# Optimization experiments

Hardware: AMD Instinct MI355X
Metric: run time of the kernel (lower is better)

## Reference

```python
import jax, jax.numpy as jnp
import numpy as np
import math

B, S, D, H = 2, 2048, 1024, 16
DK = D // H

def setup_inputs() -> dict:
    key = jax.random.key(0)
    ks = jax.random.split(key, 8)
    query = jax.random.normal(ks[0], (B, S, D), dtype=jnp.float32)
    k_in = jax.random.normal(ks[1], (B, S, D), dtype=jnp.float32)
    value = jax.random.normal(ks[2], (B, S, D), dtype=jnp.float32)
    mask = jax.random.randint(ks[3], (B, S, S), 0, 2, dtype=jnp.int32)
    scale = 1.0 / math.sqrt(D)
    Wq = jax.random.normal(ks[4], (D, D), dtype=jnp.float32) * scale
    Wk = jax.random.normal(ks[5], (D, D), dtype=jnp.float32) * scale
    Wv = jax.random.normal(ks[6], (D, D), dtype=jnp.float32) * scale
    Wo = jax.random.normal(ks[7], (D, D), dtype=jnp.float32) * scale
    return {"query": query, "key": k_in, "value": value, "mask": mask,
            "Wq": Wq, "Wk": Wk, "Wv": Wv, "Wo": Wo}

def reference(query, key, value, mask, Wq, Wk, Wv, Wo):
    # torch Linear(no bias): y = x @ W.T ; weights are [out, in]
    def split_heads(x):  # [B,S,D] -> [B,H,S,DK]
        return x.reshape(B, S, H, DK).transpose(0, 2, 1, 3)
    q = split_heads(query @ Wq.T)
    k = split_heads(key @ Wk.T)
    v = split_heads(value @ Wv.T)
    scores = jnp.einsum('bhqd,bhkd->bhqk', q, k) / jnp.sqrt(jnp.float32(DK))
    scores = jnp.where(mask[:, None, :, :] == 0, jnp.float32(-1e9), scores)
    p_attn = jax.nn.softmax(scores, axis=-1)  # dropout is identity in eval mode
    attn = jnp.einsum('bhqk,bhkd->bhqd', p_attn, v)
    out = attn.transpose(0, 2, 1, 3).reshape(B, S, D)
    return out @ Wo.T
```

## Files before the change

kernel.cpp:

```cpp
#include <hip/hip_runtime.h>
#include <hip/hip_bf16.h>
#include <cstdint>
#include <cstddef>

constexpr int BATCH = 2;
constexpr int SEQ   = 2048;
constexpr int DIM   = 1024;
constexpr int NH    = 16;
constexpr int DK    = 64;

typedef unsigned short u16;
typedef unsigned int   u32;
typedef unsigned long long u64;

typedef __attribute__((ext_vector_type(8))) short bf16x8;
typedef __attribute__((ext_vector_type(8))) unsigned short u16x8;
typedef __attribute__((ext_vector_type(4))) float f32x4;
typedef __attribute__((ext_vector_type(16))) float f32x16;
typedef __attribute__((ext_vector_type(4))) unsigned int u32x4;

__device__ __forceinline__ u16 f2bf(float f) {
  u32 u = __builtin_bit_cast(u32, f);
  u32 r = (u + 0x7FFFu + ((u >> 16) & 1u)) >> 16;
  return (u16)r;
}

__device__ __forceinline__ u32 pack_bf2(float a, float b) {
  __hip_bfloat162 h2 = __float22bfloat162_rn(make_float2(a, b));
  u32 r;
  __builtin_memcpy(&r, &h2, 4);
  return r;
}

__device__ __forceinline__ float fexp2(float x) {
#if __has_builtin(__builtin_amdgcn_exp2f)
  return __builtin_amdgcn_exp2f(x);
#else
  return exp2f(x);
#endif
}

__device__ __forceinline__ void plswap32(u32& a, u32& b) {
  asm volatile("v_permlane32_swap_b32 %0, %1" : "+v"(a), "+v"(b));
}

__device__ __forceinline__ void gload16(const u16* g, u16* l) {
  __builtin_amdgcn_global_load_lds(
      (const __attribute__((address_space(1))) void*)g,
      (__attribute__((address_space(3))) void*)l, 16, 0, 0);
}

constexpr size_t QS  = (size_t)BATCH * SEQ * DIM;
constexpr size_t WSZ = (size_t)DIM * DIM;
constexpr int CVT_BLOCKS  = (int)((3 * QS + 4 * WSZ) / (256 * 8));
constexpr int MASK_BLOCKS = (BATCH * SEQ * SEQ) / 256;

__global__ __launch_bounds__(256) void prep(const float* __restrict__ q,
                                            const float* __restrict__ k,
                                            const float* __restrict__ v,
                                            const float* __restrict__ wq,
                                            const float* __restrict__ wk,
                                            const float* __restrict__ wv,
                                            const float* __restrict__ wo,
                                            u16* __restrict__ dst,
                                            const int* __restrict__ mask,
                                            u64* __restrict__ bits) {
  const int bid = blockIdx.x;
  if (bid < CVT_BLOCKS) {
    const size_t i = ((size_t)bid * 256 + threadIdx.x) * 8;
    const float* s;
    if      (i < QS)              s = q  + i;
    else if (i < 2 * QS)          s = k  + (i - QS);
    else if (i < 3 * QS)          s = v  + (i - 2 * QS);
    else if (i < 3 * QS + WSZ)     s = wq + (i - 3 * QS);
    else if (i < 3 * QS + 2 * WSZ) s = wk + (i - 3 * QS - WSZ);
    else if (i < 3 * QS + 3 * WSZ) s = wv + (i - 3 * QS - 2 * WSZ);
    else                           s = wo + (i - 3 * QS - 3 * WSZ);
    f32x4 a = *(const f32x4*)s, b2 = *(const f32x4*)(s + 4);
    u32x4 t;
    t[0] = pack_bf2(a[0], a[1]);  t[1] = pack_bf2(a[2], a[3]);
    t[2] = pack_bf2(b2[0], b2[1]); t[3] = pack_bf2(b2[2], b2[3]);
    *(u16x8*)(dst + i) = __builtin_bit_cast(u16x8, t);
  } else {
    const int gt = (bid - CVT_BLOCKS) * 256 + threadIdx.x;
    u64 m = __ballot(mask[gt] != 0);
    if ((threadIdx.x & 63) == 0) bits[gt >> 6] = m;
  }
}

__global__ __launch_bounds__(256) void transpose_v(const u16* __restrict__ V,
                                                   u16* __restrict__ Vt) {
  __shared__ u16 t[64][68];
  const int st = blockIdx.x * 64;
  const int bh = blockIdx.y;
  const int b = bh >> 4, h = bh & 15;
  const int tid = threadIdx.x;
#pragma unroll
  for (int s = 0; s < 2; ++s) {
    int c = tid + s * 256;
    int row = c >> 3, c8 = c & 7;
    u16x8 vv = *(const u16x8*)(V + ((size_t)(b * SEQ + st + row)) * DIM + h * DK + c8 * 8);
#pragma unroll
    for (int j = 0; j < 8; ++j) t[row][c8 * 8 + j] = vv[j];
  }
  __syncthreads();
#pragma unroll
  for (int s = 0; s < 2; ++s) {
    int c = tid + s * 256;
    int dk = c >> 3, sc = c & 7;
    u16x8 ov;
#pragma unroll
    for (int j = 0; j < 8; ++j) ov[j] = t[sc * 8 + j][dk];
    *(u16x8*)(Vt + ((size_t)bh * DK + dk) * SEQ + st + sc * 8) = ov;
  }
}

struct GemmParams {
  const void* A[3];
  const void* B[3];
  void*       C[3];
  float       alpha[3];
};

template <bool OUTF32>
__global__ __launch_bounds__(256) void gemm_nt(GemmParams p, int M, int N, int K) {
  const int z = blockIdx.z;
  __shared__ __align__(16) u16 As[128 * 64];
  __shared__ __align__(16) u16 Bs[128 * 64];

  const int nbx = gridDim.x, nby = gridDim.y;
  const int lid = blockIdx.y * nbx + blockIdx.x;
  const int xcd = lid & 7, idx = lid >> 3;
  const int rows_per_xcd = nby >> 3;
  const int by = xcd * rows_per_xcd + idx / nbx;
  const int bx = idx % nbx;

  const int tid = threadIdx.x;
  const int lane = tid & 63, w = tid >> 6;
  const int l31 = lane & 31, hi = lane >> 5;
  const int bm = by * 128, bn = bx * 128;
  const int wm = (w >> 1) * 64, wn = (w & 1) * 64;

  const u16* A = (const u16*)p.A[z];
  const u16* B = (const u16*)p.B[z];

  const int srow = lane >> 3;
  const int gchk = (lane & 7) ^ srow;

  f32x16 acc[2][2] = {};

  for (int k0 = 0; k0 < K; k0 += 64) {
#pragma unroll
    for (int j = 0; j < 4; ++j) {
      const int row = 32 * w + 8 * j + srow;
      gload16(&A[(size_t)(bm + row) * K + k0 + gchk * 8], &As[2048 * w + 512 * j]);
      gload16(&B[(size_t)(bn + row) * K + k0 + gchk * 8], &Bs[2048 * w + 512 * j]);
    }
    __syncthreads();

#pragma unroll
    for (int ks = 0; ks < 4; ++ks) {
      bf16x8 af[2], bf[2];
#pragma unroll
      for (int mb = 0; mb < 2; ++mb) {
        const int row = wm + mb * 32 + l31;
        af[mb] = *(const bf16x8*)&As[row * 64 + ((2 * ks + hi) ^ (row & 7)) * 8];
      }
#pragma unroll
      for (int nb = 0; nb < 2; ++nb) {
        const int row = wn + nb * 32 + l31;
        bf[nb] = *(const bf16x8*)&Bs[row * 64 + ((2 * ks + hi) ^ (row & 7)) * 8];
      }
      __builtin_amdgcn_s_setprio(1);
#pragma unroll
      for (int mb = 0; mb < 2; ++mb)
#pragma unroll
        for (int nb = 0; nb < 2; ++nb)
          acc[mb][nb] = __builtin_amdgcn_mfma_f32_32x32x16_bf16(af[mb], bf[nb], acc[mb][nb], 0, 0, 0);
      __builtin_amdgcn_s_setprio(0);
    }
    __syncthreads();
  }

  const float alpha = p.alpha[z];
#pragma unroll
  for (int mb = 0; mb < 2; ++mb)
#pragma unroll
    for (int nb = 0; nb < 2; ++nb)
#pragma unroll
      for (int r = 0; r < 16; ++r) {
        const int row = bm + wm + mb * 32 + (r & 3) + 8 * (r >> 2) + 4 * hi;
        const int col = bn + wn + nb * 32 + l31;
        float val = acc[mb][nb][r] * alpha;
        if (OUTF32) ((float*)p.C[z])[(size_t)row * N + col] = val;
        else        ((u16*)p.C[z])[(size_t)row * N + col]  = f2bf(val);
      }
}

__global__ __launch_bounds__(512, 2) void attn_fwd(const u16* __restrict__ Qb,
                                                   const u16* __restrict__ Kb,
                                                   const u16* __restrict__ Vtb,
                                                   const u64* __restrict__ mbits,
                                                   u16* __restrict__ Ob) {
  const int h = blockIdx.y, b = blockIdx.z;
  const int tid = threadIdx.x;
  const int lane = tid & 63, w = tid >> 6;
  const int l31 = lane & 31, hi = lane >> 5;
  const int half = w >> 2, wq = w & 3;

  __shared__ __align__(16) u16 SB[2 * 16384];
  __shared__ float Lsh[4][64];

  const int q0 = blockIdx.x * 128 + wq * 32;
  const int rsw = l31 & 7;

  bf16x8 qreg[4];
  {
    const u16* qp = Qb + ((size_t)(b * SEQ + q0 + l31)) * DIM + h * DK + 8 * hi;
#pragma unroll
    for (int s = 0; s < 4; ++s) qreg[s] = *(const bf16x8*)(qp + 16 * s);
  }

  const int grow = (w << 3) + (lane >> 3);
  const int gchk = (lane & 7) ^ (grow & 7);
  const u16* kbase  = Kb + ((size_t)b * SEQ + grow) * DIM + h * DK + gchk * 8;
  const u16* vtbase = Vtb + ((size_t)(b * NH + h) * DK + grow) * SEQ + gchk * 8;
  const u64* mrow   = mbits + (size_t)(b * SEQ + q0 + l31) * (SEQ / 64) + half * 16;

  f32x16 o[2] = {};
  float lsum = 0.f;

  {
    u16* const nb = SB;
    gload16(kbase,                          nb + 0     + w * 512);
    gload16(kbase + (size_t)1024 * DIM,     nb + 4096  + w * 512);
    gload16(vtbase,                         nb + 8192  + w * 512);
    gload16(vtbase + 1024,                  nb + 12288 + w * 512);
  }
  u64 mbc = mrow[0];
  __syncthreads();

  for (int kt = 0; kt < 16; ++kt) {
    const int cur = kt & 1;
    u64 mbn = mbc;
    if (kt < 15) {
      u16* const nb = SB + (cur ^ 1) * 16384;
      const u16* ks = kbase + (size_t)(kt + 1) * 64 * DIM;
      const u16* vs = vtbase + (kt + 1) * 64;
      gload16(ks,                       nb + 0     + w * 512);
      gload16(ks + (size_t)1024 * DIM,  nb + 4096  + w * 512);
      gload16(vs,                       nb + 8192  + w * 512);
      gload16(vs + 1024,                nb + 12288 + w * 512);
      mbn = mrow[kt + 1];
    }
    const u16* const Kc = SB + cur * 16384 + half * 4096;
    const u16* const Vc = SB + cur * 16384 + 8192 + half * 4096;

    const u64 nmb = ~mbc;
    const u64 mbh = nmb >> (hi * 4);
    const u32 nm[2] = {(u32)mbh, (u32)(mbh >> 32)};
    f32x16 sc[2];
#pragma unroll
    for (int kb = 0; kb < 2; ++kb)
#pragma unroll
      for (int r = 0; r < 16; ++r) {
        const int key = (r & 3) + 8 * (r >> 2);
        u32 t = (u32)(((int)(nm[kb] << (31 - key))) >> 31) & 0xC6EA6000u;
        sc[kb][r] = __builtin_bit_cast(float, t);
      }

#pragma unroll
    for (int kb = 0; kb < 2; ++kb) {
      const int row = kb * 32 + l31;
#pragma unroll
      for (int s = 0; s < 4; ++s) {
        bf16x8 kf = *(const bf16x8*)&Kc[row * 64 + ((2 * s + hi) ^ rsw) * 8];
        sc[kb] = __builtin_amdgcn_mfma_f32_32x32x16_bf16(kf, qreg[s], sc[kb], 0, 0, 0);
      }
    }

#pragma unroll
    for (int kb = 0; kb < 2; ++kb)
#pragma unroll
      for (int r = 0; r < 16; ++r)
        sc[kb][r] = fexp2(sc[kb][r]);
    float s8[8];
#pragma unroll
    for (int i = 0; i < 8; ++i)
      s8[i] = (sc[0][i] + sc[0][i + 8]) + (sc[1][i] + sc[1][i + 8]);
    lsum += ((s8[0] + s8[1]) + (s8[2] + s8[3])) + ((s8[4] + s8[5]) + (s8[6] + s8[7]));

#pragma unroll
    for (int kb = 0; kb < 2; ++kb) {
      u32 wv[8];
#pragma unroll
      for (int t = 0; t < 8; ++t)
        wv[t] = pack_bf2(sc[kb][2 * t], sc[kb][2 * t + 1]);
      plswap32(wv[0], wv[2]);
      plswap32(wv[1], wv[3]);
      plswap32(wv[4], wv[6]);
      plswap32(wv[5], wv[7]);
      u32x4 f0 = {wv[0], wv[1], wv[2], wv[3]};
      u32x4 f1 = {wv[4], wv[5], wv[6], wv[7]};
      bf16x8 pa0 = __builtin_bit_cast(bf16x8, f0);
      bf16x8 pa1 = __builtin_bit_cast(bf16x8, f1);
#pragma unroll
      for (int ks = 0; ks < 2; ++ks) {
        bf16x8 pf = ks ? pa1 : pa0;
#pragma unroll
        for (int d = 0; d < 2; ++d) {
          const int row = l31 + 32 * d;
          bf16x8 vf = *(const bf16x8*)&Vc[row * 64 + ((4 * kb + 2 * ks + hi) ^ rsw) * 8];
          o[d] = __builtin_amdgcn_mfma_f32_32x32x16_bf16(pf, vf, o[d], 0, 0, 0);
        }
      }
    }
    mbc = mbn;
    __syncthreads();
  }

  lsum += __shfl_xor(lsum, 32, 64);
  f32x4* const oa4 = (f32x4*)SB;
  if (half == 1) {
    f32x4* dst = oa4 + (size_t)(wq * 64 + lane) * 8;
#pragma unroll
    for (int d = 0; d < 2; ++d)
#pragma unroll
      for (int cc = 0; cc < 4; ++cc) {
        f32x4 t = {o[d][cc * 4 + 0], o[d][cc * 4 + 1], o[d][cc * 4 + 2], o[d][cc * 4 + 3]};
        dst[(d * 4 + cc) ^ (lane & 7)] = t;
      }
    Lsh[wq][lane] = lsum;
  }
  __syncthreads();
  if (half == 0) {
    const float ltot = lsum + Lsh[wq][lane];
    const float linv = 1.0f / ltot;
    const f32x4* src = oa4 + (size_t)(wq * 64 + lane) * 8;
    f32x4 ov[8];
#pragma unroll
    for (int c = 0; c < 8; ++c) ov[c] = src[c ^ (lane & 7)];
    float lr[16];
#pragma unroll
    for (int r = 0; r < 16; ++r)
      lr[r] = __shfl(linv, (r & 3) + 8 * (r >> 2) + 4 * hi, 64);
#pragma unroll
    for (int d = 0; d < 2; ++d)
#pragma unroll
      for (int r = 0; r < 16; ++r) {
        const float om = o[d][r] + ov[d * 4 + (r >> 2)][r & 3];
        const int qloc = (r & 3) + 8 * (r >> 2) + 4 * hi;
        Ob[(size_t)(b * SEQ + q0 + qloc) * DIM + h * DK + l31 + 32 * d] = f2bf(om * lr[r]);
      }
  }
}

extern "C" void kernel_launch(void* const* d_in, const int* in_sizes, int n_in,
                              void* d_out, int out_size, void* d_ws, size_t ws_size,
                              hipStream_t stream) {
  const float* q    = (const float*)d_in[0];
  const float* k    = (const float*)d_in[1];
  const float* v    = (const float*)d_in[2];
  const int*   mask = (const int*)d_in[3];
  const float* Wq   = (const float*)d_in[4];
  const float* Wk   = (const float*)d_in[5];
  const float* Wv   = (const float*)d_in[6];
  const float* Wo   = (const float*)d_in[7];
  float* out = (float*)d_out;

  char* ws = (char*)d_ws;
  u64* mbits = (u64*)ws;
  u16* XB  = (u16*)(ws + 0x0100000);
  u16* xq = XB, *xk = XB + QS, *xv = XB + 2 * QS;
  u16* wqb = XB + 3 * QS, *wkb = wqb + WSZ, *wvb = wkb + WSZ, *wob = wvb + WSZ;
  u16* Qb  = (u16*)(ws + 0x2100000);
  u16* Kb  = (u16*)(ws + 0x2900000);
  u16* Vb  = (u16*)(ws + 0x3100000);
  u16* Vtb = (u16*)(ws + 0x3900000);
  u16* Ab  = (u16*)(ws + 0x4100000);

  prep<<<CVT_BLOCKS + MASK_BLOCKS, 256, 0, stream>>>(q, k, v, Wq, Wk, Wv, Wo, XB,
                                                     mask, mbits);

  GemmParams gp;
  gp.A[0] = xq;  gp.A[1] = xk;  gp.A[2] = xv;
  gp.B[0] = wqb; gp.B[1] = wkb; gp.B[2] = wvb;
  gp.C[0] = Qb;  gp.C[1] = Kb;  gp.C[2] = Vb;
  gp.alpha[0] = 0.125f * 1.44269504088896f; gp.alpha[1] = 1.0f; gp.alpha[2] = 1.0f;
  gemm_nt<false><<<dim3(DIM / 128, (BATCH * SEQ) / 128, 3), 256, 0, stream>>>(
      gp, BATCH * SEQ, DIM, DIM);

  transpose_v<<<dim3(SEQ / 64, BATCH * NH), 256, 0, stream>>>(Vb, Vtb);

  attn_fwd<<<dim3(SEQ / 128, NH, BATCH), 512, 0, stream>>>(Qb, Kb, Vtb, mbits, Ab);

  GemmParams go;
  go.A[0] = Ab; go.B[0] = wob; go.C[0] = out; go.alpha[0] = 1.0f;
  go.A[1] = go.A[2] = nullptr; go.B[1] = go.B[2] = nullptr; go.C[1] = go.C[2] = nullptr;
  go.alpha[1] = go.alpha[2] = 1.0f;
  gemm_nt<true><<<dim3(DIM / 128, (BATCH * SEQ) / 128, 1), 256, 0, stream>>>(
      go, BATCH * SEQ, DIM, DIM);
}
```

Measured before the change: 136.5 us.

## Single-buffer V tile, load it during QK and softmax, add mid-iteration barrier

V is no longer double-buffered. Each iteration issues the current V tile's global-to-LDS loads at its start and adds a barrier before the PV MFMAs, so the load overlaps QK^T and exp within the same iteration. This reduces LDS from 64KB to 48KB per block and the launch bound asks for more blocks per CU, in exchange for an extra barrier per iteration and less latency hiding for V. The mask-bit expansion also switches to a signed bitfield-extract builtin.

```diff
diff --git a/kernel.cpp b/kernel.cpp
--- a/kernel.cpp
+++ b/kernel.cpp
@@ -37,6 +37,14 @@
   return __builtin_amdgcn_exp2f(x);
 #else
   return exp2f(x);
+#endif
+}
+
+__device__ __forceinline__ u32 bit_to_allones(u32 word, int bit) {
+#if __has_builtin(__builtin_amdgcn_sbfe)
+  return (u32)__builtin_amdgcn_sbfe((int)word, bit, 1);
+#else
+  return (u32)(((int)(word << (31 - bit))) >> 31);
 #endif
 }
 
@@ -197,7 +205,7 @@
       }
 }
 
-__global__ __launch_bounds__(512, 2) void attn_fwd(const u16* __restrict__ Qb,
+__global__ __launch_bounds__(512, 8) void attn_fwd(const u16* __restrict__ Qb,
                                                    const u16* __restrict__ Kb,
                                                    const u16* __restrict__ Vtb,
                                                    const u64* __restrict__ mbits,
@@ -208,7 +216,8 @@
   const int l31 = lane & 31, hi = lane >> 5;
   const int half = w >> 2, wq = w & 3;
 
-  __shared__ __align__(16) u16 SB[2 * 16384];
+  __shared__ __align__(16) u16 Kbuf[2][8192];
+  __shared__ __align__(16) u16 Vbuf[8192];
   __shared__ float Lsh[4][64];
 
   const int q0 = blockIdx.x * 128 + wq * 32;
@@ -230,31 +239,25 @@
   f32x16 o[2] = {};
   float lsum = 0.f;
 
-  {
-    u16* const nb = SB;
-    gload16(kbase,                          nb + 0     + w * 512);
-    gload16(kbase + (size_t)1024 * DIM,     nb + 4096  + w * 512);
-    gload16(vtbase,                         nb + 8192  + w * 512);
-    gload16(vtbase + 1024,                  nb + 12288 + w * 512);
-  }
+  gload16(kbase,                      &Kbuf[0][0]    + w * 512);
+  gload16(kbase + (size_t)1024 * DIM, &Kbuf[0][4096] + w * 512);
   u64 mbc = mrow[0];
   __syncthreads();
 
   for (int kt = 0; kt < 16; ++kt) {
     const int cur = kt & 1;
+
+    gload16(vtbase + kt * 64,                      &Vbuf[0]    + w * 512);
+    gload16(vtbase + 1024 + kt * 64,               &Vbuf[4096] + w * 512);
     u64 mbn = mbc;
     if (kt < 15) {
-      u16* const nb = SB + (cur ^ 1) * 16384;
       const u16* ks = kbase + (size_t)(kt + 1) * 64 * DIM;
-      const u16* vs = vtbase + (kt + 1) * 64;
-      gload16(ks,                       nb + 0     + w * 512);
-      gload16(ks + (size_t)1024 * DIM,  nb + 4096  + w * 512);
-      gload16(vs,                       nb + 8192  + w * 512);
-      gload16(vs + 1024,                nb + 12288 + w * 512);
+      gload16(ks,                       &Kbuf[cur ^ 1][0]    + w * 512);
+      gload16(ks + (size_t)1024 * DIM,  &Kbuf[cur ^ 1][4096] + w * 512);
       mbn = mrow[kt + 1];
     }
-    const u16* const Kc = SB + cur * 16384 + half * 4096;
-    const u16* const Vc = SB + cur * 16384 + 8192 + half * 4096;
+    const u16* const Kc = &Kbuf[cur][half * 4096];
+    const u16* const Vc = &Vbuf[half * 4096];
 
     const u64 nmb = ~mbc;
     const u64 mbh = nmb >> (hi * 4);
@@ -265,7 +268,7 @@
 #pragma unroll
       for (int r = 0; r < 16; ++r) {
         const int key = (r & 3) + 8 * (r >> 2);
-        u32 t = (u32)(((int)(nm[kb] << (31 - key))) >> 31) & 0xC6EA6000u;
+        u32 t = bit_to_allones(nm[kb], key) & 0xC6EA6000u;
         sc[kb][r] = __builtin_bit_cast(float, t);
       }
 
@@ -290,6 +293,7 @@
       s8[i] = (sc[0][i] + sc[0][i + 8]) + (sc[1][i] + sc[1][i + 8]);
     lsum += ((s8[0] + s8[1]) + (s8[2] + s8[3])) + ((s8[4] + s8[5]) + (s8[6] + s8[7]));
 
+    bf16x8 pa[2][2];
 #pragma unroll
     for (int kb = 0; kb < 2; ++kb) {
       u32 wv[8];
@@ -302,11 +306,17 @@
       plswap32(wv[5], wv[7]);
       u32x4 f0 = {wv[0], wv[1], wv[2], wv[3]};
       u32x4 f1 = {wv[4], wv[5], wv[6], wv[7]};
-      bf16x8 pa0 = __builtin_bit_cast(bf16x8, f0);
-      bf16x8 pa1 = __builtin_bit_cast(bf16x8, f1);
+      pa[kb][0] = __builtin_bit_cast(bf16x8, f0);
+      pa[kb][1] = __builtin_bit_cast(bf16x8, f1);
+    }
+
+    __syncthreads();
+
+#pragma unroll
+    for (int kb = 0; kb < 2; ++kb)
 #pragma unroll
       for (int ks = 0; ks < 2; ++ks) {
-        bf16x8 pf = ks ? pa1 : pa0;
+        bf16x8 pf = pa[kb][ks];
 #pragma unroll
         for (int d = 0; d < 2; ++d) {
           const int row = l31 + 32 * d;
@@ -314,13 +324,12 @@
           o[d] = __builtin_amdgcn_mfma_f32_32x32x16_bf16(pf, vf, o[d], 0, 0, 0);
         }
       }
-    }
     mbc = mbn;
     __syncthreads();
   }
 
   lsum += __shfl_xor(lsum, 32, 64);
-  f32x4* const oa4 = (f32x4*)SB;
+  f32x4* const oa4 = (f32x4*)&Kbuf[0][0];
   if (half == 1) {
     f32x4* dst = oa4 + (size_t)(wq * 64 + lane) * 8;
 #pragma unroll
```

After: 146.4 us. +7.3%, slower.
